# Optimization experiments

Measured on AMD Instinct MI355X. Metric: run time of the kernel, lower is better.

Reference implementation:

```python
import jax, jax.numpy as jnp
import numpy as np

DISTANCE_SCALE = 25.0
VIEW_PE = 6
STEP = 0.02  # nominal ray-march step size used to scale dists


def positional_encoding(positions, freqs):
    # matches torch: (positions[..., None] * 2**k).reshape(..., freqs*C) -> [sin, cos]
    freq_bands = 2.0 ** jnp.arange(freqs, dtype=positions.dtype)
    pts = (positions[..., None] * freq_bands).reshape(positions.shape[:-1] + (freqs * positions.shape[-1],))
    return jnp.concatenate([jnp.sin(pts), jnp.cos(pts)], axis=-1)


def setup_inputs() -> dict:
    key = jax.random.key(0)
    ks = jax.random.split(key, 10)
    n_rays, n_samples, C, featureC = 4096, 256, 27, 128
    in_mlpC = 3 + 2 * VIEW_PE * 3 + C  # 66
    density_features = jax.random.normal(ks[0], (n_rays, n_samples), jnp.float32)
    app_features = jax.random.normal(ks[1], (n_rays, n_samples, C), jnp.float32)
    viewdirs = jax.random.normal(ks[2], (n_rays, 3), jnp.float32)
    viewdirs = viewdirs / jnp.linalg.norm(viewdirs, axis=-1, keepdims=True)
    dists = jax.random.uniform(ks[3], (n_rays, n_samples), jnp.float32) * STEP
    s1 = 1.0 / np.sqrt(in_mlpC)
    s2 = 1.0 / np.sqrt(featureC)
    W1 = jax.random.uniform(ks[4], (in_mlpC, featureC), jnp.float32, -s1, s1)
    b1 = jax.random.uniform(ks[5], (featureC,), jnp.float32, -s1, s1)
    W2 = jax.random.uniform(ks[6], (featureC, featureC), jnp.float32, -s2, s2)
    b2 = jax.random.uniform(ks[7], (featureC,), jnp.float32, -s2, s2)
    W3 = jax.random.uniform(ks[8], (featureC, 3), jnp.float32, -s2, s2)
    b3 = jnp.zeros((3,), jnp.float32)  # torch init: constant_(bias, 0)
    return {"density_features": density_features, "app_features": app_features,
            "viewdirs": viewdirs, "dists": dists,
            "W1": W1, "b1": b1, "W2": W2, "b2": b2, "W3": W3, "b3": b3}


def reference(density_features, app_features, viewdirs, dists, W1, b1, W2, b2, W3, b3):
    # feature2density (relu activation)
    sigma = jax.nn.relu(density_features)  # [R, S]
    # raw2alpha
    alpha = 1.0 - jnp.exp(-sigma * dists * DISTANCE_SCALE)  # [R, S]
    T = jnp.cumprod(jnp.concatenate([jnp.ones((alpha.shape[0], 1), alpha.dtype),
                                     1.0 - alpha + 1e-10], axis=-1), axis=-1)
    weights = alpha * T[:, :-1]  # [R, S]
    # radiance MLP over all sample points
    R, S, C = app_features.shape
    vd = jnp.broadcast_to(viewdirs[:, None, :], (R, S, 3))
    mlp_in = jnp.concatenate([app_features, vd, positional_encoding(vd, VIEW_PE)], axis=-1)  # [R,S,66]
    h = jax.nn.relu(mlp_in @ W1 + b1)
    h = jax.nn.relu(h @ W2 + b2)
    rgb = jax.nn.sigmoid(h @ W3 + b3)  # [R, S, 3]
    # composite (white background)
    acc_map = jnp.sum(weights, axis=-1)  # [R]
    rgb_map = jnp.einsum('rs,rsc->rc', weights, rgb)  # [R, 3]
    rgb_map = jnp.clip(rgb_map + (1.0 - acc_map[:, None]), 0.0, 1.0)
    return rgb_map
```

## Files before the change

kernel.cpp:

```cpp
#include <hip/hip_runtime.h>
#include <hip/hip_bf16.h>

typedef float f32x4 __attribute__((ext_vector_type(4)));
typedef short s16x8 __attribute__((ext_vector_type(8)));
typedef unsigned int u32;
typedef u32 u32x2 __attribute__((ext_vector_type(2)));

#define DIST_SCALE 25.0f

__device__ __forceinline__ unsigned short f2b(float f) {
  union { float f; unsigned u; } v; v.f = f;
  unsigned r = v.u + 0x7fffu + ((v.u >> 16) & 1u);
  return (unsigned short)(r >> 16);
}

__device__ __forceinline__ u32 cvtpk(float lo, float hi) {
  u32 r;
  asm("v_cvt_pk_bf16_f32 %0, %1, %2" : "=v"(r) : "v"(lo), "v"(hi));
  return r;
}

__global__ void prep_weights(const float* __restrict__ W1, const float* __restrict__ W2,
                             const float* __restrict__ W3, unsigned short* __restrict__ ws) {
  int t = blockIdx.x * 256 + threadIdx.x;
  int stride = gridDim.x * 256;
  for (int i = t; i < 128 * 32; i += stride) {
    int n = i >> 5, k = i & 31;
    ws[i] = (k < 27) ? f2b(W1[k * 128 + n]) : (unsigned short)0;
  }
  unsigned short* w2t = ws + 4096;
  for (int i = t; i < 128 * 128; i += stride) {
    int n = i >> 7, k = i & 127;
    w2t[i] = f2b(W2[k * 128 + n]);
  }
  unsigned short* w3p = ws + 4096 + 16384;
  for (int i = t; i < 4 * 16 * 32; i += stride) {
    int wv = i >> 9, rem = i & 511, n = rem >> 5, ks = rem & 31;
    int kg = ks >> 3, j = ks & 7;
    int ch = wv * 32 + ((j >> 2) << 4) + kg * 4 + (j & 3);
    w3p[i] = (n < 3) ? f2b(W3[ch * 3 + n]) : (unsigned short)0;
  }
}

__global__ void __launch_bounds__(256) nerf_main(
    const float* __restrict__ dens, const float* __restrict__ app,
    const float* __restrict__ vdirs, const float* __restrict__ dists,
    const float* __restrict__ W1, const float* __restrict__ b1,
    const float* __restrict__ b2v, const float* __restrict__ b3v,
    const unsigned short* __restrict__ wsb, float* __restrict__ out) {
  __shared__ unsigned short HA[2 * 64 * 128];
  __shared__ __align__(16) float part[2 * 64 * 12];
  __shared__ float wbuf[256];
  __shared__ float hcbuf[128];
  __shared__ float featbuf[40];
  __shared__ float red[4][4];

  const int t = threadIdx.x;
  const int lane = t & 63;
  const int wv = t >> 6;
  const int r = blockIdx.x;

  const unsigned short* W1aT = wsb;
  const unsigned short* W2T = wsb + 4096;
  const unsigned short* W3P = wsb + 4096 + 16384;
  char* HAb = (char*)HA;
  char* partB = (char*)part;
  char* hcB = (char*)hcbuf;

  const int cl = lane & 15;
  const int kg = lane >> 4;
  const int chBase = wv * 32;
  const int myS = wv * 16 + cl;

  const float* rayBase = app + (size_t)r * 6912;

  f32x4 va, vb;
  {
    const float* gp = rayBase + myS * 27 + kg * 8;
    va = *(const f32x4*)gp;
    vb = *(const f32x4*)(gp + 4);
  }

  const u32 swzw = (u32)((myS & 7) << 4);
  const u32 swzr = (u32)((cl & 7) << 4);
  u32 wo[8];
#pragma unroll
  for (int nt = 0; nt < 8; ++nt)
    wo[nt] = (u32)(myS * 256) + (((u32)(nt * 32 + kg * 8)) ^ swzw);
  u32 ro[4];
#pragma unroll
  for (int kk = 0; kk < 4; ++kk)
    ro[kk] = (u32)(cl * 256) + (((u32)(kk * 64 + kg * 16)) ^ swzr);
  const u32 po_w = (u32)(cl * 48 + wv * 4);
  const u32 po_r = (u32)(myS * 48 + kg * 16);
  const u32 ho = (u32)(kg * 16);

  if (t < 39) {
    float val;
    if (t < 3) val = vdirs[r * 3 + t];
    else {
      int jj = t - 3;
      int trig = jj / 18;
      int rem = jj % 18;
      int c = rem / 6, k = rem % 6;
      float v = vdirs[r * 3 + c] * (float)(1 << k);
      val = trig ? cosf(v) : sinf(v);
    }
    featbuf[t] = val;
  }
  if (wv == 0) {
    const float4 dv = *(const float4*)(dens + (size_t)r * 256 + lane * 4);
    const float4 tv = *(const float4*)(dists + (size_t)r * 256 + lane * 4);
    float f[4], al[4];
    float dl[4] = {dv.x, dv.y, dv.z, dv.w};
    float tl[4] = {tv.x, tv.y, tv.z, tv.w};
    float p = 1.0f;
#pragma unroll
    for (int q = 0; q < 4; ++q) {
      float sg = fmaxf(dl[q], 0.0f);
      float e = __expf(-sg * tl[q] * DIST_SCALE);
      al[q] = 1.0f - e;
      f[q] = e + 1e-10f;
      p *= f[q];
    }
    float P = p;
#pragma unroll
    for (int dlt = 1; dlt < 64; dlt <<= 1) {
      float v = __shfl_up(P, dlt, 64);
      if (lane >= dlt) P *= v;
    }
    float E = __shfl_up(P, 1, 64);
    if (lane == 0) E = 1.0f;
    float tr = E;
#pragma unroll
    for (int q = 0; q < 4; ++q) { wbuf[lane * 4 + q] = al[q] * tr; tr *= f[q]; }
  }
  __syncthreads();
  if (t < 128) {
    float s = b1[t];
    for (int j = 0; j < 39; ++j) s += featbuf[j] * W1[(27 + j) * 128 + t];
    hcbuf[t] = s;
  }

  s16x8 w1f[8], w2f[2][4], w3s;
#pragma unroll
  for (int nt = 0; nt < 8; ++nt)
    w1f[nt] = *(const s16x8*)(W1aT + (nt * 16 + cl) * 32 + kg * 8);
#pragma unroll
  for (int nt = 0; nt < 2; ++nt)
#pragma unroll
    for (int kk = 0; kk < 4; ++kk)
      w2f[nt][kk] = *(const s16x8*)(W2T + (chBase + nt * 16 + cl) * 128 + kk * 32 + kg * 8);
  w3s = *(const s16x8*)(W3P + wv * 512 + cl * 32 + kg * 8);

  const f32x4 bb0 = *(const f32x4*)(b2v + chBase + kg * 4);
  const f32x4 bb1 = *(const f32x4*)(b2v + chBase + 16 + kg * 4);
  const float b3c = (kg < 3) ? b3v[kg] : 0.0f;
  float pacc = 0.0f;

  __syncthreads();

#pragma unroll
  for (int chunk = 0; chunk < 4; ++chunk) {
    const int HB = (chunk & 1) * 16384;

    {
      union { u32 u[4]; s16x8 v; } xb;
      xb.u[0] = cvtpk(va[0], va[1]);
      xb.u[1] = cvtpk(va[2], va[3]);
      xb.u[2] = cvtpk(vb[0], vb[1]);
      xb.u[3] = cvtpk(vb[2], vb[3]);
#pragma unroll
      for (int nt = 0; nt < 8; ++nt) {
        f32x4 hcf = *(const f32x4*)(hcB + ho + nt * 64);
        f32x4 a = hcf;
        a = __builtin_amdgcn_mfma_f32_16x16x32_bf16(w1f[nt], xb.v, a, 0, 0, 0);
        u32x2 pk = {cvtpk(fmaxf(a[0], 0.0f), fmaxf(a[1], 0.0f)),
                    cvtpk(fmaxf(a[2], 0.0f), fmaxf(a[3], 0.0f))};
        *(u32x2*)(HAb + wo[nt] + HB) = pk;
      }
    }

    if (chunk < 3) {
      const float* gp = rayBase + (chunk + 1) * 1728 + myS * 27 + kg * 8;
      if (__builtin_expect(r == 4095 && chunk == 2 && myS == 63 && kg == 3, 0)) {
        va = (f32x4){gp[0], gp[1], gp[2], 0.0f};
        vb = (f32x4){0.0f, 0.0f, 0.0f, 0.0f};
      } else {
        va = *(const f32x4*)gp;
        vb = *(const f32x4*)(gp + 4);
      }
    }

    __syncthreads();

    if (chunk > 0) {
      const float w = wbuf[(chunk - 1) * 64 + myS];
      if (kg < 3) {
        f32x4 pv = *(const f32x4*)(partB + po_r + ((chunk - 1) & 1) * 3072);
        float v = (pv[0] + pv[1]) + (pv[2] + pv[3]) + b3c;
        pacc += w / (1.0f + __expf(-v));
      } else {
        pacc += w;
      }
    }

#pragma unroll
    for (int st = 0; st < 4; ++st) {
      s16x8 hbf[4];
#pragma unroll
      for (int kk = 0; kk < 4; ++kk)
        hbf[kk] = *(const s16x8*)(HAb + ro[kk] + HB + st * 4096);
      f32x4 a0 = bb0, a1 = bb1;
#pragma unroll
      for (int kk = 0; kk < 4; ++kk) {
        a0 = __builtin_amdgcn_mfma_f32_16x16x32_bf16(w2f[0][kk], hbf[kk], a0, 0, 0, 0);
        a1 = __builtin_amdgcn_mfma_f32_16x16x32_bf16(w2f[1][kk], hbf[kk], a1, 0, 0, 0);
      }
      union { u32 u[4]; s16x8 v; } b3;
      b3.u[0] = cvtpk(fmaxf(a0[0], 0.0f), fmaxf(a0[1], 0.0f));
      b3.u[1] = cvtpk(fmaxf(a0[2], 0.0f), fmaxf(a0[3], 0.0f));
      b3.u[2] = cvtpk(fmaxf(a1[0], 0.0f), fmaxf(a1[1], 0.0f));
      b3.u[3] = cvtpk(fmaxf(a1[2], 0.0f), fmaxf(a1[3], 0.0f));
      f32x4 p3 = {};
      p3 = __builtin_amdgcn_mfma_f32_16x16x32_bf16(w3s, b3.v, p3, 0, 0, 0);
      if (kg == 0) {
        char* pw = partB + po_w + (chunk & 1) * 3072 + st * 768;
        *(float*)(pw) = p3[0];
        *(float*)(pw + 16) = p3[1];
        *(float*)(pw + 32) = p3[2];
      }
    }
  }

  __syncthreads();
  {
    const float w = wbuf[3 * 64 + myS];
    if (kg < 3) {
      f32x4 pv = *(const f32x4*)(partB + po_r + 3072);
      float v = (pv[0] + pv[1]) + (pv[2] + pv[3]) + b3c;
      pacc += w / (1.0f + __expf(-v));
    } else {
      pacc += w;
    }
  }
#pragma unroll
  for (int d = 1; d < 16; d <<= 1) pacc += __shfl_xor(pacc, d, 64);
  if (cl == 0) red[wv][kg] = pacc;
  __syncthreads();
  if (t == 0) {
    float R = red[0][0] + red[1][0] + red[2][0] + red[3][0];
    float G = red[0][1] + red[1][1] + red[2][1] + red[3][1];
    float B = red[0][2] + red[1][2] + red[2][2] + red[3][2];
    float W = red[0][3] + red[1][3] + red[2][3] + red[3][3];
    float bg = 1.0f - W;
    out[r * 3 + 0] = fminf(fmaxf(R + bg, 0.0f), 1.0f);
    out[r * 3 + 1] = fminf(fmaxf(G + bg, 0.0f), 1.0f);
    out[r * 3 + 2] = fminf(fmaxf(B + bg, 0.0f), 1.0f);
  }
}

extern "C" void kernel_launch(void* const* d_in, const int* in_sizes, int n_in,
                              void* d_out, int out_size, void* d_ws, size_t ws_size,
                              hipStream_t stream) {
  const float* dens = (const float*)d_in[0];
  const float* app  = (const float*)d_in[1];
  const float* vd   = (const float*)d_in[2];
  const float* dist = (const float*)d_in[3];
  const float* W1   = (const float*)d_in[4];
  const float* b1   = (const float*)d_in[5];
  const float* W2   = (const float*)d_in[6];
  const float* b2   = (const float*)d_in[7];
  const float* W3   = (const float*)d_in[8];
  const float* b3   = (const float*)d_in[9];
  unsigned short* wsb = (unsigned short*)d_ws;

  prep_weights<<<32, 256, 0, stream>>>(W1, W2, W3, wsb);
  nerf_main<<<4096, 256, 0, stream>>>(dens, app, vd, dist, W1, b1, b2, b3, wsb, (float*)d_out);
}
```

Before: 77.28 us.

## Permute W2 K-order to allow 16-byte LDS stores of layer-1 output

Reorders the K dimension of the packed W2 so that two adjacent layer-1 output tiles can be written to LDS as a single 128-bit store instead of two 64-bit stores, with matching permutation in weight prep. Hoists the layer-1 bias/viewdir contribution (hcbuf) into registers once instead of reloading from LDS every chunk. Adds s_setprio around the layer-2 MFMA block to favor matrix issue across waves. Costs extra registers (32 floats for hcf) which may pressure occupancy.

```diff
diff --git a/kernel.cpp b/kernel.cpp
--- a/kernel.cpp
+++ b/kernel.cpp
@@ -4,7 +4,7 @@
 typedef float f32x4 __attribute__((ext_vector_type(4)));
 typedef short s16x8 __attribute__((ext_vector_type(8)));
 typedef unsigned int u32;
-typedef u32 u32x2 __attribute__((ext_vector_type(2)));
+typedef u32 u32x4 __attribute__((ext_vector_type(4)));
 
 #define DIST_SCALE 25.0f
 
@@ -28,10 +28,11 @@
     int n = i >> 5, k = i & 31;
     ws[i] = (k < 27) ? f2b(W1[k * 128 + n]) : (unsigned short)0;
   }
-  unsigned short* w2t = ws + 4096;
+  unsigned short* w2q = ws + 4096;
   for (int i = t; i < 128 * 128; i += stride) {
-    int n = i >> 7, k = i & 127;
-    w2t[i] = f2b(W2[k * 128 + n]);
+    int n = i >> 7, q = i & 127;
+    int ch = (2 * (q >> 5) + ((q >> 2) & 1)) * 16 + ((q >> 3) & 3) * 4 + (q & 3);
+    w2q[i] = f2b(W2[ch * 128 + n]);
   }
   unsigned short* w3p = ws + 4096 + 16384;
   for (int i = t; i < 4 * 16 * 32; i += stride) {
@@ -61,11 +62,10 @@
   const int r = blockIdx.x;
 
   const unsigned short* W1aT = wsb;
-  const unsigned short* W2T = wsb + 4096;
+  const unsigned short* W2Q = wsb + 4096;
   const unsigned short* W3P = wsb + 4096 + 16384;
   char* HAb = (char*)HA;
   char* partB = (char*)part;
-  char* hcB = (char*)hcbuf;
 
   const int cl = lane & 15;
   const int kg = lane >> 4;
@@ -83,17 +83,16 @@
 
   const u32 swzw = (u32)((myS & 7) << 4);
   const u32 swzr = (u32)((cl & 7) << 4);
-  u32 wo[8];
-#pragma unroll
-  for (int nt = 0; nt < 8; ++nt)
-    wo[nt] = (u32)(myS * 256) + (((u32)(nt * 32 + kg * 8)) ^ swzw);
+  u32 wo4[4];
+#pragma unroll
+  for (int ntp = 0; ntp < 4; ++ntp)
+    wo4[ntp] = (u32)(myS * 256) + (((u32)(ntp * 64 + kg * 16)) ^ swzw);
   u32 ro[4];
 #pragma unroll
   for (int kk = 0; kk < 4; ++kk)
     ro[kk] = (u32)(cl * 256) + (((u32)(kk * 64 + kg * 16)) ^ swzr);
   const u32 po_w = (u32)(cl * 48 + wv * 4);
   const u32 po_r = (u32)(myS * 48 + kg * 16);
-  const u32 ho = (u32)(kg * 16);
 
   if (t < 39) {
     float val;
@@ -150,7 +149,7 @@
   for (int nt = 0; nt < 2; ++nt)
 #pragma unroll
     for (int kk = 0; kk < 4; ++kk)
-      w2f[nt][kk] = *(const s16x8*)(W2T + (chBase + nt * 16 + cl) * 128 + kk * 32 + kg * 8);
+      w2f[nt][kk] = *(const s16x8*)(W2Q + (chBase + nt * 16 + cl) * 128 + kk * 32 + kg * 8);
   w3s = *(const s16x8*)(W3P + wv * 512 + cl * 32 + kg * 8);
 
   const f32x4 bb0 = *(const f32x4*)(b2v + chBase + kg * 4);
@@ -159,6 +158,11 @@
   float pacc = 0.0f;
 
   __syncthreads();
+
+  f32x4 hcf[8];
+#pragma unroll
+  for (int nt = 0; nt < 8; ++nt)
+    hcf[nt] = *(const f32x4*)(hcbuf + nt * 16 + kg * 4);
 
 #pragma unroll
   for (int chunk = 0; chunk < 4; ++chunk) {
@@ -171,13 +175,15 @@
       xb.u[2] = cvtpk(vb[0], vb[1]);
       xb.u[3] = cvtpk(vb[2], vb[3]);
 #pragma unroll
-      for (int nt = 0; nt < 8; ++nt) {
-        f32x4 hcf = *(const f32x4*)(hcB + ho + nt * 64);
-        f32x4 a = hcf;
-        a = __builtin_amdgcn_mfma_f32_16x16x32_bf16(w1f[nt], xb.v, a, 0, 0, 0);
-        u32x2 pk = {cvtpk(fmaxf(a[0], 0.0f), fmaxf(a[1], 0.0f)),
-                    cvtpk(fmaxf(a[2], 0.0f), fmaxf(a[3], 0.0f))};
-        *(u32x2*)(HAb + wo[nt] + HB) = pk;
+      for (int ntp = 0; ntp < 4; ++ntp) {
+        f32x4 a0 = hcf[2 * ntp], a1 = hcf[2 * ntp + 1];
+        a0 = __builtin_amdgcn_mfma_f32_16x16x32_bf16(w1f[2 * ntp], xb.v, a0, 0, 0, 0);
+        a1 = __builtin_amdgcn_mfma_f32_16x16x32_bf16(w1f[2 * ntp + 1], xb.v, a1, 0, 0, 0);
+        u32x4 pk = {cvtpk(fmaxf(a0[0], 0.0f), fmaxf(a0[1], 0.0f)),
+                    cvtpk(fmaxf(a0[2], 0.0f), fmaxf(a0[3], 0.0f)),
+                    cvtpk(fmaxf(a1[0], 0.0f), fmaxf(a1[1], 0.0f)),
+                    cvtpk(fmaxf(a1[2], 0.0f), fmaxf(a1[3], 0.0f))};
+        *(u32x4*)(HAb + wo4[ntp] + HB) = pk;
       }
     }
 
@@ -212,11 +218,13 @@
       for (int kk = 0; kk < 4; ++kk)
         hbf[kk] = *(const s16x8*)(HAb + ro[kk] + HB + st * 4096);
       f32x4 a0 = bb0, a1 = bb1;
+      __builtin_amdgcn_s_setprio(1);
 #pragma unroll
       for (int kk = 0; kk < 4; ++kk) {
         a0 = __builtin_amdgcn_mfma_f32_16x16x32_bf16(w2f[0][kk], hbf[kk], a0, 0, 0, 0);
         a1 = __builtin_amdgcn_mfma_f32_16x16x32_bf16(w2f[1][kk], hbf[kk], a1, 0, 0, 0);
       }
+      __builtin_amdgcn_s_setprio(0);
       union { u32 u[4]; s16x8 v; } b3;
       b3.u[0] = cvtpk(fmaxf(a0[0], 0.0f), fmaxf(a0[1], 0.0f));
       b3.u[1] = cvtpk(fmaxf(a0[2], 0.0f), fmaxf(a0[3], 0.0f));
```

New measurement: 75.52 us. 2.3% less time.
